# Performance work log

Hardware: AMD Instinct MI355X
Metric: run time of the kernel (lower is better)

The kernel has to match this reference:

```python
import jax, jax.numpy as jnp
import numpy as np

NUM_HEADS = 4
LOCAL_RADIUS = 2


def setup_inputs() -> dict:
    key = jax.random.key(0)
    ks = jax.random.split(key, 7)
    B, C, H, W = 1, 256, 40, 40
    O = 256  # out_channels
    s = 1.0 / np.sqrt(C).astype(np.float32)
    x = jax.random.normal(ks[0], (B, C, H, W), dtype=jnp.float32)
    Wq = jax.random.normal(ks[1], (C, O), dtype=jnp.float32) * s
    Wk = jax.random.normal(ks[2], (C, O), dtype=jnp.float32) * s
    Wv = jax.random.normal(ks[3], (C, O), dtype=jnp.float32) * s
    bq = jnp.zeros((O,), jnp.float32)
    bk = jnp.zeros((O,), jnp.float32)
    bv = jnp.zeros((O,), jnp.float32)
    return {"x": x, "Wq": Wq, "bq": bq, "Wk": Wk, "bk": bk, "Wv": Wv, "bv": bv}


def reference(x, Wq, bq, Wk, bk, Wv, bv):
    B, C, H, W = x.shape
    N = H * W
    O = Wq.shape[1]
    hd = O // NUM_HEADS
    # Faithful to torch: x.view(B, N, -1) is a raw row-major reshape of (B,C,H,W)
    xf = x.reshape(B, N, C)
    # projections -> (B, heads, N, head_dim)
    q = (xf @ Wq + bq).reshape(B, N, NUM_HEADS, hd).transpose(0, 2, 1, 3)
    k = (xf @ Wk + bk).reshape(B, N, NUM_HEADS, hd).transpose(0, 2, 1, 3)
    v = (xf @ Wv + bv).reshape(B, N, NUM_HEADS, hd).transpose(0, 2, 1, 3)
    scale = jnp.asarray(O, jnp.float32) ** 0.5
    acc = jnp.zeros_like(v)
    # 25 shifted full-attention passes; roll is over (heads, points) axes,
    # exactly matching torch key.roll(shifts=(h,w), dims=(-3,-2)).
    for h in range(-LOCAL_RADIUS, LOCAL_RADIUS + 1):
        for w in range(-LOCAL_RADIUS, LOCAL_RADIUS + 1):
            rk = jnp.roll(k, shift=(h, w), axis=(1, 2))
            scores = jnp.einsum('bhnd,bhmd->bhnm', q, rk) / scale  # (B,h,N,N)
            attn = jax.nn.softmax(scores, axis=-1)
            rv = jnp.roll(v, shift=(-h, -w), axis=(1, 2))
            acc = acc + jnp.einsum('bhnm,bhmd->bhnd', attn, rv)
    # (B, heads, N, hd) -> (B, N, O)
    return acc.transpose(0, 2, 1, 3).reshape(B, N, O)
```

## Files before the change

kernel.cpp:

```cpp
#include <hip/hip_runtime.h>
#include <hip/hip_bf16.h>
#include <stdint.h>

typedef __attribute__((ext_vector_type(8))) __bf16 bf16x8;
typedef __attribute__((ext_vector_type(4))) float f32x4;

#define N_PTS 1600
#define HD    64

#define OFF_WT   0u
#define OFF_BIAS 393216u
#define OFF_VHT  394752u
#define OFF_QH   1213952u
#define OFF_KH   2033152u
#define OFF_KF   2852352u
#define OFF_VF   3671552u

__device__ __forceinline__ float bf2f(ushort h) {
  union { uint32_t u; float f; } v; v.u = ((uint32_t)h) << 16; return v.f;
}
__device__ __forceinline__ ushort f2bf(float f) {
  union { float f; uint32_t u; } v; v.f = f;
  uint32_t u = v.u;
  return (ushort)((u + 0x7FFFu + ((u >> 16) & 1u)) >> 16);
}
__device__ __forceinline__ uint32_t pk2(float a, float b) {
  union { __hip_bfloat162 h; uint32_t u; } cv;
  cv.h = __float22bfloat162_rn(make_float2(a, b));
  return cv.u;
}

__device__ __forceinline__ int detect_f32(const ushort* xu, int* shflag) {
  int t = threadIdx.x & 255;
  if (t == 0) *shflag = 0;
  __syncthreads();
  int local = 0;
#pragma unroll
  for (int i = 0; i < 4; ++i) {
    float v = bf2f(xu[(t * 4 + i) * 2]);
    if (!(fabsf(v) < 1e4f)) local = 1;
  }
  if (local) atomicOr(shflag, 1);
  __syncthreads();
  return *shflag;
}

__global__ void k_prep(const void* __restrict__ x, const void* __restrict__ Wq,
                       const void* __restrict__ bq, const void* __restrict__ Wk,
                       const void* __restrict__ bk, const void* __restrict__ Wv,
                       const void* __restrict__ bv, char* __restrict__ ws) {
  __shared__ int shflag;
  __shared__ ushort tileb[32][33];
  int isf32 = detect_f32((const ushort*)x, &shflag);
  int b = blockIdx.x, t = threadIdx.x;

  if (b < 192) {
    int z = b >> 6, tile = b & 63;
    const void* W = (z == 0) ? Wq : ((z == 1) ? Wk : Wv);
    int o0 = (tile & 7) * 32, k0 = (tile >> 3) * 32;
    int tx = t & 31, ty = t >> 5;
#pragma unroll
    for (int i = 0; i < 32; i += 8) {
      int kk = (k0 + ty + i) * 256 + o0 + tx;
      tileb[ty + i][tx] = isf32 ? f2bf(((const float*)W)[kk]) : ((const ushort*)W)[kk];
    }
    __syncthreads();
    ushort* WT = (ushort*)(ws + OFF_WT) + z * 65536;
#pragma unroll
    for (int i = 0; i < 32; i += 8)
      WT[(o0 + ty + i) * 256 + k0 + tx] = tileb[tx][ty + i];
  } else {
    ushort* bb = (ushort*)(ws + OFF_BIAS);
#pragma unroll
    for (int z = 0; z < 3; ++z) {
      const void* B = (z == 0) ? bq : ((z == 1) ? bk : bv);
      bb[z * 256 + t] = isf32 ? f2bf(((const float*)B)[t]) : ((const ushort*)B)[t];
    }
  }
}

__launch_bounds__(256)
__global__ void k_proj(const void* __restrict__ x, const ushort* __restrict__ WT,
                       const ushort* __restrict__ bias3,
                       ushort* __restrict__ Qh, ushort* __restrict__ Kh, ushort* __restrict__ VhT) {
  __shared__ int shflag;
  int isf32 = detect_f32((const ushort*)x, &shflag);
  int z = blockIdx.z;
  const ushort* WTz = WT + z * 65536;
  const ushort* bias = bias3 + z * 256;
  int n0 = blockIdx.x * 16;
  int head = threadIdx.x >> 6;
  int lane = threadIdx.x & 63;
  int c = lane & 15, quad = lane >> 4;

  f32x4 acc[4];
#pragma unroll
  for (int i = 0; i < 4; ++i) acc[i] = (f32x4){0.f, 0.f, 0.f, 0.f};

  int ebase = (n0 + c) * 256;
#pragma unroll
  for (int kt = 0; kt < 8; ++kt) {
    bf16x8 a;
    if (isf32) {
      const float4* X4 = (const float4*)x;
      int i4 = (ebase + kt * 32 + quad * 8) >> 2;
      float4 f0 = X4[i4], f1 = X4[i4 + 1];
      union { ushort us[8]; bf16x8 v; } cv;
      cv.us[0] = f2bf(f0.x); cv.us[1] = f2bf(f0.y);
      cv.us[2] = f2bf(f0.z); cv.us[3] = f2bf(f0.w);
      cv.us[4] = f2bf(f1.x); cv.us[5] = f2bf(f1.y);
      cv.us[6] = f2bf(f1.z); cv.us[7] = f2bf(f1.w);
      a = cv.v;
    } else {
      a = *(const bf16x8*)((const ushort*)x + ebase + kt * 32 + quad * 8);
    }
#pragma unroll
    for (int os = 0; os < 4; ++os) {
      bf16x8 bfr = *(const bf16x8*)(WTz + (head * 64 + os * 16 + c) * 256 + kt * 32 + quad * 8);
      acc[os] = __builtin_amdgcn_mfma_f32_16x16x32_bf16(a, bfr, acc[os], 0, 0, 0);
    }
  }
  if (z == 2) {
#pragma unroll
    for (int os = 0; os < 4; ++os) {
      float bval = bf2f(bias[head * 64 + os * 16 + c]);
      ushort4 v;
      v.x = f2bf(acc[os][0] + bval); v.y = f2bf(acc[os][1] + bval);
      v.z = f2bf(acc[os][2] + bval); v.w = f2bf(acc[os][3] + bval);
      *(ushort4*)(VhT + (head * 64 + os * 16 + c) * N_PTS + n0 + quad * 4) = v;
    }
  } else {
    float scale = (z == 0) ? 0.0625f * 1.44269504088896f : 1.0f;
    ushort* out = (z == 0) ? Qh : Kh;
#pragma unroll
    for (int os = 0; os < 4; ++os) {
      float bval = bf2f(bias[head * 64 + os * 16 + c]);
#pragma unroll
      for (int r = 0; r < 4; ++r)
        out[head * (N_PTS * HD) + (n0 + quad * 4 + r) * HD + os * 16 + c] =
            f2bf((acc[os][r] + bval) * scale);
    }
  }
}

__global__ void k_frag(const ushort* __restrict__ Kh, const ushort* __restrict__ VhT,
                       ushort* __restrict__ Kf, ushort* __restrict__ Vf) {
  int q = blockIdx.x * 256 + threadIdx.x;
  int isV = q >= 51200;
  int idx = isV ? q - 51200 : q;
  int lane = idx & 63, ch = (idx >> 6) & 3;
  int rest = idx >> 8;
  int t = rest % 50, g = rest / 50;
  int c = lane & 15, quad = lane >> 4;
  if (!isV) {
    int perm = ((c >> 2) << 3) + (c & 3);
    int key = t * 32 + perm + ((ch >> 1) << 2);
    int d0 = (ch & 1) * 32 + quad * 8;
    bf16x8 v = *(const bf16x8*)(Kh + (size_t)(g * N_PTS + key) * HD + d0);
    *(bf16x8*)(Kf + (size_t)idx * 8) = v;
  } else {
    int d = ch * 16 + c;
    int m0 = t * 32 + quad * 8;
    const ushort* row = VhT + (size_t)(g * HD + d) * N_PTS;
    int mp = (m0 == 0) ? 1592 : m0 - 8;
    int mn = (m0 == 1592) ? 0 : m0 + 8;
    union { bf16x8 v[3]; ushort us[24]; } w;
    w.v[0] = *(const bf16x8*)(row + mp);
    w.v[1] = *(const bf16x8*)(row + m0);
    w.v[2] = *(const bf16x8*)(row + mn);
    union { ushort us[8]; bf16x8 v; } o;
#pragma unroll
    for (int j = 0; j < 8; ++j) {
      float s = bf2f(w.us[4 + j]) + bf2f(w.us[6 + j]) + bf2f(w.us[8 + j]) +
                bf2f(w.us[10 + j]) + bf2f(w.us[12 + j]);
      o.us[j] = f2bf(s);
    }
    *(bf16x8*)(Vf + (size_t)idx * 8) = o.v;
  }
}

__device__ __forceinline__ bf16x8 pack_p8(const f32x4& s0, const f32x4& s1, float& lp) {
  float e0 = exp2f(s0[0]), e1 = exp2f(s0[1]), e2 = exp2f(s0[2]), e3 = exp2f(s0[3]);
  float e4 = exp2f(s1[0]), e5 = exp2f(s1[1]), e6 = exp2f(s1[2]), e7 = exp2f(s1[3]);
  lp += ((e0 + e1) + (e2 + e3)) + ((e4 + e5) + (e6 + e7));
  union { uint32_t u[4]; bf16x8 v; } r;
  r.u[0] = pk2(e0, e1); r.u[1] = pk2(e2, e3);
  r.u[2] = pk2(e4, e5); r.u[3] = pk2(e6, e7);
  return r.v;
}

#define MFMA16(a, b, cc) __builtin_amdgcn_mfma_f32_16x16x32_bf16(a, b, cc, 0, 0, 0)

#define LOADT(sfx, t) do {                                            \
    const char* kt_ = kfp + (size_t)(t) * 4096;                       \
    const char* vt_ = vfp + (size_t)(t) * 4096;                       \
    ka0##sfx = *(const bf16x8*)(kt_);                                 \
    ka1##sfx = *(const bf16x8*)(kt_ + 1024);                          \
    kb0##sfx = *(const bf16x8*)(kt_ + 2048);                          \
    kb1##sfx = *(const bf16x8*)(kt_ + 3072);                          \
    vb0##sfx = *(const bf16x8*)(vt_);                                 \
    vb1##sfx = *(const bf16x8*)(vt_ + 1024);                          \
    vb2##sfx = *(const bf16x8*)(vt_ + 2048);                          \
    vb3##sfx = *(const bf16x8*)(vt_ + 3072);                          \
  } while (0)

#define COMPUTE(sfx) do {                                             \
    __builtin_amdgcn_s_setprio(1);                                    \
    f32x4 s0 = MFMA16(ka0##sfx, qa00, z4);                            \
    s0 = MFMA16(ka1##sfx, qa01, s0);                                  \
    f32x4 s1 = MFMA16(kb0##sfx, qa00, z4);                            \
    s1 = MFMA16(kb1##sfx, qa01, s1);                                  \
    bf16x8 pa0 = pack_p8(s0, s1, lp0);                                \
    oacc0[0] = MFMA16(pa0, vb0##sfx, oacc0[0]);                       \
    oacc0[1] = MFMA16(pa0, vb1##sfx, oacc0[1]);                       \
    oacc0[2] = MFMA16(pa0, vb2##sfx, oacc0[2]);                       \
    oacc0[3] = MFMA16(pa0, vb3##sfx, oacc0[3]);                       \
    s0 = MFMA16(ka0##sfx, qa10, z4);                                  \
    s0 = MFMA16(ka1##sfx, qa11, s0);                                  \
    s1 = MFMA16(kb0##sfx, qa10, z4);                                  \
    s1 = MFMA16(kb1##sfx, qa11, s1);                                  \
    bf16x8 pa1 = pack_p8(s0, s1, lp1);                                \
    oacc1[0] = MFMA16(pa1, vb0##sfx, oacc1[0]);                       \
    oacc1[1] = MFMA16(pa1, vb1##sfx, oacc1[1]);                       \
    oacc1[2] = MFMA16(pa1, vb2##sfx, oacc1[2]);                       \
    oacc1[3] = MFMA16(pa1, vb3##sfx, oacc1[3]);                       \
    __builtin_amdgcn_s_setprio(0);                                    \
  } while (0)

__launch_bounds__(512)
__global__ void k_attn(const ushort* __restrict__ Qh, const ushort* __restrict__ Kf,
                       const ushort* __restrict__ Vf, const void* __restrict__ x,
                       void* __restrict__ out) {
  __shared__ int shflag;
  __shared__ float obuf[8][16][68];
  __shared__ float lbuf[8][16];
  int isf32 = detect_f32((const ushort*)x, &shflag);

  int qt = blockIdx.x;
  int hp = blockIdx.y;
  int tid = threadIdx.x, sp = tid >> 6, lane = tid & 63;
  int kg = sp & 3, zh = sp >> 2;
  int vg = (2 * hp - kg + 8) & 3;
  int c = lane & 15, quad = lane >> 4;
  int n0 = qt * 16;

  const ushort* q0row = Qh + ((hp    ) * N_PTS + n0 + c) * HD;
  const ushort* q1row = Qh + ((hp + 2) * N_PTS + n0 + c) * HD;
  bf16x8 qa00 = *(const bf16x8*)(q0row + quad * 8);
  bf16x8 qa01 = *(const bf16x8*)(q0row + 32 + quad * 8);
  bf16x8 qa10 = *(const bf16x8*)(q1row + quad * 8);
  bf16x8 qa11 = *(const bf16x8*)(q1row + 32 + quad * 8);

  f32x4 oacc0[4], oacc1[4];
#pragma unroll
  for (int i = 0; i < 4; ++i) {
    oacc0[i] = (f32x4){0.f, 0.f, 0.f, 0.f};
    oacc1[i] = (f32x4){0.f, 0.f, 0.f, 0.f};
  }
  float lp0 = 0.f, lp1 = 0.f;

  int off = zh * 25;
  const int iters = 25;
  const f32x4 z4 = (f32x4){0.f, 0.f, 0.f, 0.f};

  const char* kfp = (const char*)Kf + (size_t)(kg * 50 + off) * 4096 + lane * 16;
  const char* vfp = (const char*)Vf + (size_t)(vg * 50 + off) * 4096 + lane * 16;

  bf16x8 ka0A, ka1A, kb0A, kb1A, vb0A, vb1A, vb2A, vb3A;
  bf16x8 ka0B, ka1B, kb0B, kb1B, vb0B, vb1B, vb2B, vb3B;

  LOADT(A, 0);
  int it = 0;
  for (; it + 2 <= iters; it += 2) {
    LOADT(B, it + 1);
    COMPUTE(A);
    int tn = (it + 2 < iters) ? (it + 2) : (it + 1);
    LOADT(A, tn);
    COMPUTE(B);
  }
  if (it < iters) COMPUTE(A);

  lp0 += __shfl_xor(lp0, 16, 64); lp0 += __shfl_xor(lp0, 32, 64);
  lp1 += __shfl_xor(lp1, 16, 64); lp1 += __shfl_xor(lp1, 32, 64);

#pragma unroll
  for (int h = 0; h < 2; ++h) {
    __syncthreads();
    const f32x4* oa = h ? oacc1 : oacc0;
#pragma unroll
    for (int ds = 0; ds < 4; ++ds)
#pragma unroll
      for (int r = 0; r < 4; ++r)
        obuf[sp][quad * 4 + r][ds * 16 + c] = oa[ds][r];
    if (quad == 0) lbuf[sp][c] = h ? lp1 : lp0;
    __syncthreads();

    int q = tid >> 5, dp = (tid & 31) * 2;
    int hq = hp + 2 * h;
    float a0 = 0.f, a1 = 0.f;
#pragma unroll
    for (int g = 0; g < 4; ++g) {
      float n0v = obuf[g][q][dp]     + obuf[g + 4][q][dp];
      float n1v = obuf[g][q][dp + 1] + obuf[g + 4][q][dp + 1];
      float l   = lbuf[g][q] + lbuf[g + 4][q];
      float w   = (g == ((hq + 2) & 3)) ? 2.f : 1.f;
      float rl  = w / l;
      a0 += n0v * rl; a1 += n1v * rl;
    }
    size_t oidx = (size_t)(n0 + q) * 256 + hq * 64 + dp;
    if (isf32) {
      ((float2*)out)[oidx >> 1] = make_float2(a0, a1);
    } else {
      ((uint32_t*)out)[oidx >> 1] = pk2(a0, a1);
    }
  }
}

extern "C" void kernel_launch(void* const* d_in, const int* in_sizes, int n_in,
                              void* d_out, int out_size, void* d_ws, size_t ws_size,
                              hipStream_t stream) {
  char* ws = (char*)d_ws;
  ushort* WT    = (ushort*)(ws + OFF_WT);
  ushort* bias3 = (ushort*)(ws + OFF_BIAS);
  ushort* VhT   = (ushort*)(ws + OFF_VHT);
  ushort* Qh    = (ushort*)(ws + OFF_QH);
  ushort* Kh    = (ushort*)(ws + OFF_KH);
  ushort* Kf    = (ushort*)(ws + OFF_KF);
  ushort* Vf    = (ushort*)(ws + OFF_VF);

  k_prep<<<193, 256, 0, stream>>>(d_in[0], d_in[1], d_in[2], d_in[3],
                                  d_in[4], d_in[5], d_in[6], ws);
  k_proj<<<dim3(100, 1, 3), 256, 0, stream>>>(d_in[0], WT, bias3, Qh, Kh, VhT);
  k_frag<<<400, 256, 0, stream>>>(Kh, VhT, Kf, Vf);
  k_attn<<<dim3(100, 2), 512, 0, stream>>>(Qh, Kf, Vf, d_in[0], d_out);
}
```

Baseline: 109.4 us.

## Fuse prep, projection, fragment and attention kernels into one cooperative kernel

Replaces four separate kernel launches with a single cooperative launch of 200 blocks of 512 threads, using grid-wide syncs between the weight transpose, QKV projection, K/V fragment reshuffle and attention phases. Each phase's work is remapped onto the fixed grid: 512-thread blocks split into two 256-thread halves for projection jobs, and each block handles 512 fragment elements. This removes launch overheads and inter-kernel gaps. The cost is grid-barrier latency and a larger shared-memory footprint per block, which applies across every phase.

Measured after the change: 192.9 us. 1.76x slower.

```diff
diff --git a/kernel.cpp b/kernel.cpp
--- a/kernel.cpp
+++ b/kernel.cpp
@@ -1,6 +1,9 @@
 #include <hip/hip_runtime.h>
 #include <hip/hip_bf16.h>
+#include <hip/hip_cooperative_groups.h>
 #include <stdint.h>
+
+namespace cg = cooperative_groups;
 
 typedef __attribute__((ext_vector_type(8))) __bf16 bf16x8;
 typedef __attribute__((ext_vector_type(4))) float f32x4;
@@ -43,140 +46,6 @@
   if (local) atomicOr(shflag, 1);
   __syncthreads();
   return *shflag;
-}
-
-__global__ void k_prep(const void* __restrict__ x, const void* __restrict__ Wq,
-                       const void* __restrict__ bq, const void* __restrict__ Wk,
-                       const void* __restrict__ bk, const void* __restrict__ Wv,
-                       const void* __restrict__ bv, char* __restrict__ ws) {
-  __shared__ int shflag;
-  __shared__ ushort tileb[32][33];
-  int isf32 = detect_f32((const ushort*)x, &shflag);
-  int b = blockIdx.x, t = threadIdx.x;
-
-  if (b < 192) {
-    int z = b >> 6, tile = b & 63;
-    const void* W = (z == 0) ? Wq : ((z == 1) ? Wk : Wv);
-    int o0 = (tile & 7) * 32, k0 = (tile >> 3) * 32;
-    int tx = t & 31, ty = t >> 5;
-#pragma unroll
-    for (int i = 0; i < 32; i += 8) {
-      int kk = (k0 + ty + i) * 256 + o0 + tx;
-      tileb[ty + i][tx] = isf32 ? f2bf(((const float*)W)[kk]) : ((const ushort*)W)[kk];
-    }
-    __syncthreads();
-    ushort* WT = (ushort*)(ws + OFF_WT) + z * 65536;
-#pragma unroll
-    for (int i = 0; i < 32; i += 8)
-      WT[(o0 + ty + i) * 256 + k0 + tx] = tileb[tx][ty + i];
-  } else {
-    ushort* bb = (ushort*)(ws + OFF_BIAS);
-#pragma unroll
-    for (int z = 0; z < 3; ++z) {
-      const void* B = (z == 0) ? bq : ((z == 1) ? bk : bv);
-      bb[z * 256 + t] = isf32 ? f2bf(((const float*)B)[t]) : ((const ushort*)B)[t];
-    }
-  }
-}
-
-__launch_bounds__(256)
-__global__ void k_proj(const void* __restrict__ x, const ushort* __restrict__ WT,
-                       const ushort* __restrict__ bias3,
-                       ushort* __restrict__ Qh, ushort* __restrict__ Kh, ushort* __restrict__ VhT) {
-  __shared__ int shflag;
-  int isf32 = detect_f32((const ushort*)x, &shflag);
-  int z = blockIdx.z;
-  const ushort* WTz = WT + z * 65536;
-  const ushort* bias = bias3 + z * 256;
-  int n0 = blockIdx.x * 16;
-  int head = threadIdx.x >> 6;
-  int lane = threadIdx.x & 63;
-  int c = lane & 15, quad = lane >> 4;
-
-  f32x4 acc[4];
-#pragma unroll
-  for (int i = 0; i < 4; ++i) acc[i] = (f32x4){0.f, 0.f, 0.f, 0.f};
-
-  int ebase = (n0 + c) * 256;
-#pragma unroll
-  for (int kt = 0; kt < 8; ++kt) {
-    bf16x8 a;
-    if (isf32) {
-      const float4* X4 = (const float4*)x;
-      int i4 = (ebase + kt * 32 + quad * 8) >> 2;
-      float4 f0 = X4[i4], f1 = X4[i4 + 1];
-      union { ushort us[8]; bf16x8 v; } cv;
-      cv.us[0] = f2bf(f0.x); cv.us[1] = f2bf(f0.y);
-      cv.us[2] = f2bf(f0.z); cv.us[3] = f2bf(f0.w);
-      cv.us[4] = f2bf(f1.x); cv.us[5] = f2bf(f1.y);
-      cv.us[6] = f2bf(f1.z); cv.us[7] = f2bf(f1.w);
-      a = cv.v;
-    } else {
-      a = *(const bf16x8*)((const ushort*)x + ebase + kt * 32 + quad * 8);
-    }
-#pragma unroll
-    for (int os = 0; os < 4; ++os) {
-      bf16x8 bfr = *(const bf16x8*)(WTz + (head * 64 + os * 16 + c) * 256 + kt * 32 + quad * 8);
-      acc[os] = __builtin_amdgcn_mfma_f32_16x16x32_bf16(a, bfr, acc[os], 0, 0, 0);
-    }
-  }
-  if (z == 2) {
-#pragma unroll
-    for (int os = 0; os < 4; ++os) {
-      float bval = bf2f(bias[head * 64 + os * 16 + c]);
-      ushort4 v;
-      v.x = f2bf(acc[os][0] + bval); v.y = f2bf(acc[os][1] + bval);
-      v.z = f2bf(acc[os][2] + bval); v.w = f2bf(acc[os][3] + bval);
-      *(ushort4*)(VhT + (head * 64 + os * 16 + c) * N_PTS + n0 + quad * 4) = v;
-    }
-  } else {
-    float scale = (z == 0) ? 0.0625f * 1.44269504088896f : 1.0f;
-    ushort* out = (z == 0) ? Qh : Kh;
-#pragma unroll
-    for (int os = 0; os < 4; ++os) {
-      float bval = bf2f(bias[head * 64 + os * 16 + c]);
-#pragma unroll
-      for (int r = 0; r < 4; ++r)
-        out[head * (N_PTS * HD) + (n0 + quad * 4 + r) * HD + os * 16 + c] =
-            f2bf((acc[os][r] + bval) * scale);
-    }
-  }
-}
-
-__global__ void k_frag(const ushort* __restrict__ Kh, const ushort* __restrict__ VhT,
-                       ushort* __restrict__ Kf, ushort* __restrict__ Vf) {
-  int q = blockIdx.x * 256 + threadIdx.x;
-  int isV = q >= 51200;
-  int idx = isV ? q - 51200 : q;
-  int lane = idx & 63, ch = (idx >> 6) & 3;
-  int rest = idx >> 8;
-  int t = rest % 50, g = rest / 50;
-  int c = lane & 15, quad = lane >> 4;
-  if (!isV) {
-    int perm = ((c >> 2) << 3) + (c & 3);
-    int key = t * 32 + perm + ((ch >> 1) << 2);
-    int d0 = (ch & 1) * 32 + quad * 8;
-    bf16x8 v = *(const bf16x8*)(Kh + (size_t)(g * N_PTS + key) * HD + d0);
-    *(bf16x8*)(Kf + (size_t)idx * 8) = v;
-  } else {
-    int d = ch * 16 + c;
-    int m0 = t * 32 + quad * 8;
-    const ushort* row = VhT + (size_t)(g * HD + d) * N_PTS;
-    int mp = (m0 == 0) ? 1592 : m0 - 8;
-    int mn = (m0 == 1592) ? 0 : m0 + 8;
-    union { bf16x8 v[3]; ushort us[24]; } w;
-    w.v[0] = *(const bf16x8*)(row + mp);
-    w.v[1] = *(const bf16x8*)(row + m0);
-    w.v[2] = *(const bf16x8*)(row + mn);
-    union { ushort us[8]; bf16x8 v; } o;
-#pragma unroll
-    for (int j = 0; j < 8; ++j) {
-      float s = bf2f(w.us[4 + j]) + bf2f(w.us[6 + j]) + bf2f(w.us[8 + j]) +
-                bf2f(w.us[10 + j]) + bf2f(w.us[12 + j]);
-      o.us[j] = f2bf(s);
-    }
-    *(bf16x8*)(Vf + (size_t)idx * 8) = o.v;
-  }
 }
 
 __device__ __forceinline__ bf16x8 pack_p8(const f32x4& s0, const f32x4& s1, float& lp) {
@@ -228,90 +97,231 @@
   } while (0)
 
 __launch_bounds__(512)
-__global__ void k_attn(const ushort* __restrict__ Qh, const ushort* __restrict__ Kf,
-                       const ushort* __restrict__ Vf, const void* __restrict__ x,
-                       void* __restrict__ out) {
+__global__ void k_fused(const void* __restrict__ x, const void* __restrict__ Wq,
+                        const void* __restrict__ bq, const void* __restrict__ Wk,
+                        const void* __restrict__ bk, const void* __restrict__ Wv,
+                        const void* __restrict__ bv, char* __restrict__ ws,
+                        void* __restrict__ out) {
+  cg::grid_group grid = cg::this_grid();
   __shared__ int shflag;
+  __shared__ ushort tileb[32][33];
   __shared__ float obuf[8][16][68];
   __shared__ float lbuf[8][16];
+
   int isf32 = detect_f32((const ushort*)x, &shflag);
-
-  int qt = blockIdx.x;
-  int hp = blockIdx.y;
-  int tid = threadIdx.x, sp = tid >> 6, lane = tid & 63;
-  int kg = sp & 3, zh = sp >> 2;
-  int vg = (2 * hp - kg + 8) & 3;
-  int c = lane & 15, quad = lane >> 4;
-  int n0 = qt * 16;
-
-  const ushort* q0row = Qh + ((hp    ) * N_PTS + n0 + c) * HD;
-  const ushort* q1row = Qh + ((hp + 2) * N_PTS + n0 + c) * HD;
-  bf16x8 qa00 = *(const bf16x8*)(q0row + quad * 8);
-  bf16x8 qa01 = *(const bf16x8*)(q0row + 32 + quad * 8);
-  bf16x8 qa10 = *(const bf16x8*)(q1row + quad * 8);
-  bf16x8 qa11 = *(const bf16x8*)(q1row + 32 + quad * 8);
-
-  f32x4 oacc0[4], oacc1[4];
-#pragma unroll
-  for (int i = 0; i < 4; ++i) {
-    oacc0[i] = (f32x4){0.f, 0.f, 0.f, 0.f};
-    oacc1[i] = (f32x4){0.f, 0.f, 0.f, 0.f};
-  }
-  float lp0 = 0.f, lp1 = 0.f;
-
-  int off = zh * 25;
-  const int iters = 25;
-  const f32x4 z4 = (f32x4){0.f, 0.f, 0.f, 0.f};
-
-  const char* kfp = (const char*)Kf + (size_t)(kg * 50 + off) * 4096 + lane * 16;
-  const char* vfp = (const char*)Vf + (size_t)(vg * 50 + off) * 4096 + lane * 16;
-
-  bf16x8 ka0A, ka1A, kb0A, kb1A, vb0A, vb1A, vb2A, vb3A;
-  bf16x8 ka0B, ka1B, kb0B, kb1B, vb0B, vb1B, vb2B, vb3B;
-
-  LOADT(A, 0);
-  int it = 0;
-  for (; it + 2 <= iters; it += 2) {
-    LOADT(B, it + 1);
-    COMPUTE(A);
-    int tn = (it + 2 < iters) ? (it + 2) : (it + 1);
-    LOADT(A, tn);
-    COMPUTE(B);
-  }
-  if (it < iters) COMPUTE(A);
-
-  lp0 += __shfl_xor(lp0, 16, 64); lp0 += __shfl_xor(lp0, 32, 64);
-  lp1 += __shfl_xor(lp1, 16, 64); lp1 += __shfl_xor(lp1, 32, 64);
-
-#pragma unroll
-  for (int h = 0; h < 2; ++h) {
+  int b = blockIdx.x, tid = threadIdx.x;
+
+  if (b < 192) {
+    int z = b >> 6, tile = b & 63;
+    const void* W = (z == 0) ? Wq : ((z == 1) ? Wk : Wv);
+    int o0 = (tile & 7) * 32, k0 = (tile >> 3) * 32;
+    int tx = tid & 31, ty = tid >> 5;
+#pragma unroll
+    for (int i = 0; i < 32; i += 16) {
+      int kk = (k0 + ty + i) * 256 + o0 + tx;
+      tileb[ty + i][tx] = isf32 ? f2bf(((const float*)W)[kk]) : ((const ushort*)W)[kk];
+    }
     __syncthreads();
-    const f32x4* oa = h ? oacc1 : oacc0;
-#pragma unroll
-    for (int ds = 0; ds < 4; ++ds)
-#pragma unroll
-      for (int r = 0; r < 4; ++r)
-        obuf[sp][quad * 4 + r][ds * 16 + c] = oa[ds][r];
-    if (quad == 0) lbuf[sp][c] = h ? lp1 : lp0;
-    __syncthreads();
-
-    int q = tid >> 5, dp = (tid & 31) * 2;
-    int hq = hp + 2 * h;
-    float a0 = 0.f, a1 = 0.f;
-#pragma unroll
-    for (int g = 0; g < 4; ++g) {
-      float n0v = obuf[g][q][dp]     + obuf[g + 4][q][dp];
-      float n1v = obuf[g][q][dp + 1] + obuf[g + 4][q][dp + 1];
-      float l   = lbuf[g][q] + lbuf[g + 4][q];
-      float w   = (g == ((hq + 2) & 3)) ? 2.f : 1.f;
-      float rl  = w / l;
-      a0 += n0v * rl; a1 += n1v * rl;
-    }
-    size_t oidx = (size_t)(n0 + q) * 256 + hq * 64 + dp;
-    if (isf32) {
-      ((float2*)out)[oidx >> 1] = make_float2(a0, a1);
+    ushort* WT = (ushort*)(ws + OFF_WT) + z * 65536;
+#pragma unroll
+    for (int i = 0; i < 32; i += 16)
+      WT[(o0 + ty + i) * 256 + k0 + tx] = tileb[tx][ty + i];
+  } else if (b == 192 && tid < 256) {
+    ushort* bb = (ushort*)(ws + OFF_BIAS);
+#pragma unroll
+    for (int z = 0; z < 3; ++z) {
+      const void* B = (z == 0) ? bq : ((z == 1) ? bk : bv);
+      bb[z * 256 + tid] = isf32 ? f2bf(((const float*)B)[tid]) : ((const ushort*)B)[tid];
+    }
+  }
+  grid.sync();
+
+  {
+    int half = tid >> 8;
+    int job = b + 200 * half;
+    if (job < 300) {
+      int z = job / 100;
+      int n0 = (job % 100) * 16;
+      const ushort* WTz = (const ushort*)(ws + OFF_WT) + z * 65536;
+      const ushort* bias = (const ushort*)(ws + OFF_BIAS) + z * 256;
+      int t256 = tid & 255;
+      int head = t256 >> 6, lane = t256 & 63;
+      int c = lane & 15, quad = lane >> 4;
+
+      f32x4 acc[4];
+#pragma unroll
+      for (int i = 0; i < 4; ++i) acc[i] = (f32x4){0.f, 0.f, 0.f, 0.f};
+
+      int ebase = (n0 + c) * 256;
+#pragma unroll
+      for (int kt = 0; kt < 8; ++kt) {
+        bf16x8 a;
+        if (isf32) {
+          const float4* X4 = (const float4*)x;
+          int i4 = (ebase + kt * 32 + quad * 8) >> 2;
+          float4 f0 = X4[i4], f1 = X4[i4 + 1];
+          union { ushort us[8]; bf16x8 v; } cv;
+          cv.us[0] = f2bf(f0.x); cv.us[1] = f2bf(f0.y);
+          cv.us[2] = f2bf(f0.z); cv.us[3] = f2bf(f0.w);
+          cv.us[4] = f2bf(f1.x); cv.us[5] = f2bf(f1.y);
+          cv.us[6] = f2bf(f1.z); cv.us[7] = f2bf(f1.w);
+          a = cv.v;
+        } else {
+          a = *(const bf16x8*)((const ushort*)x + ebase + kt * 32 + quad * 8);
+        }
+#pragma unroll
+        for (int os = 0; os < 4; ++os) {
+          bf16x8 bfr = *(const bf16x8*)(WTz + (head * 64 + os * 16 + c) * 256 + kt * 32 + quad * 8);
+          acc[os] = __builtin_amdgcn_mfma_f32_16x16x32_bf16(a, bfr, acc[os], 0, 0, 0);
+        }
+      }
+      if (z == 2) {
+        ushort* VhT = (ushort*)(ws + OFF_VHT);
+#pragma unroll
+        for (int os = 0; os < 4; ++os) {
+          float bval = bf2f(bias[head * 64 + os * 16 + c]);
+          ushort4 v;
+          v.x = f2bf(acc[os][0] + bval); v.y = f2bf(acc[os][1] + bval);
+          v.z = f2bf(acc[os][2] + bval); v.w = f2bf(acc[os][3] + bval);
+          *(ushort4*)(VhT + (head * 64 + os * 16 + c) * N_PTS + n0 + quad * 4) = v;
+        }
+      } else {
+        float scale = (z == 0) ? 0.0625f * 1.44269504088896f : 1.0f;
+        ushort* o = (ushort*)(ws + ((z == 0) ? OFF_QH : OFF_KH));
+#pragma unroll
+        for (int os = 0; os < 4; ++os) {
+          float bval = bf2f(bias[head * 64 + os * 16 + c]);
+#pragma unroll
+          for (int r = 0; r < 4; ++r)
+            o[head * (N_PTS * HD) + (n0 + quad * 4 + r) * HD + os * 16 + c] =
+                f2bf((acc[os][r] + bval) * scale);
+        }
+      }
+    }
+  }
+  grid.sync();
+
+  {
+    const ushort* Kh = (const ushort*)(ws + OFF_KH);
+    const ushort* VhT = (const ushort*)(ws + OFF_VHT);
+    ushort* Kf = (ushort*)(ws + OFF_KF);
+    ushort* Vf = (ushort*)(ws + OFF_VF);
+    int q = b * 512 + tid;
+    int isV = q >= 51200;
+    int idx = isV ? q - 51200 : q;
+    int lane = idx & 63, ch = (idx >> 6) & 3;
+    int rest = idx >> 8;
+    int t = rest % 50, g = rest / 50;
+    int c = lane & 15, quad = lane >> 4;
+    if (!isV) {
+      int perm = ((c >> 2) << 3) + (c & 3);
+      int key = t * 32 + perm + ((ch >> 1) << 2);
+      int d0 = (ch & 1) * 32 + quad * 8;
+      bf16x8 v = *(const bf16x8*)(Kh + (size_t)(g * N_PTS + key) * HD + d0);
+      *(bf16x8*)(Kf + (size_t)idx * 8) = v;
     } else {
-      ((uint32_t*)out)[oidx >> 1] = pk2(a0, a1);
+      int d = ch * 16 + c;
+      int m0 = t * 32 + quad * 8;
+      const ushort* row = VhT + (size_t)(g * HD + d) * N_PTS;
+      int mp = (m0 == 0) ? 1592 : m0 - 8;
+      int mn = (m0 == 1592) ? 0 : m0 + 8;
+      union { bf16x8 v[3]; ushort us[24]; } w;
+      w.v[0] = *(const bf16x8*)(row + mp);
+      w.v[1] = *(const bf16x8*)(row + m0);
+      w.v[2] = *(const bf16x8*)(row + mn);
+      union { ushort us[8]; bf16x8 v; } o;
+#pragma unroll
+      for (int j = 0; j < 8; ++j) {
+        float s = bf2f(w.us[4 + j]) + bf2f(w.us[6 + j]) + bf2f(w.us[8 + j]) +
+                  bf2f(w.us[10 + j]) + bf2f(w.us[12 + j]);
+        o.us[j] = f2bf(s);
+      }
+      *(bf16x8*)(Vf + (size_t)idx * 8) = o.v;
+    }
+  }
+  grid.sync();
+
+  {
+    const ushort* Qh = (const ushort*)(ws + OFF_QH);
+    const char* Kf = (const char*)(ws + OFF_KF);
+    const char* Vf = (const char*)(ws + OFF_VF);
+    int hp = (b >= 100) ? 1 : 0;
+    int qt = b - hp * 100;
+    int sp = tid >> 6, lane = tid & 63;
+    int kg = sp & 3, zh = sp >> 2;
+    int vg = (2 * hp - kg + 8) & 3;
+    int c = lane & 15, quad = lane >> 4;
+    int n0 = qt * 16;
+
+    const ushort* q0row = Qh + ((hp    ) * N_PTS + n0 + c) * HD;
+    const ushort* q1row = Qh + ((hp + 2) * N_PTS + n0 + c) * HD;
+    bf16x8 qa00 = *(const bf16x8*)(q0row + quad * 8);
+    bf16x8 qa01 = *(const bf16x8*)(q0row + 32 + quad * 8);
+    bf16x8 qa10 = *(const bf16x8*)(q1row + quad * 8);
+    bf16x8 qa11 = *(const bf16x8*)(q1row + 32 + quad * 8);
+
+    f32x4 oacc0[4], oacc1[4];
+#pragma unroll
+    for (int i = 0; i < 4; ++i) {
+      oacc0[i] = (f32x4){0.f, 0.f, 0.f, 0.f};
+      oacc1[i] = (f32x4){0.f, 0.f, 0.f, 0.f};
+    }
+    float lp0 = 0.f, lp1 = 0.f;
+
+    int off = zh * 25;
+    const int iters = 25;
+    const f32x4 z4 = (f32x4){0.f, 0.f, 0.f, 0.f};
+
+    const char* kfp = Kf + (size_t)(kg * 50 + off) * 4096 + lane * 16;
+    const char* vfp = Vf + (size_t)(vg * 50 + off) * 4096 + lane * 16;
+
+    bf16x8 ka0A, ka1A, kb0A, kb1A, vb0A, vb1A, vb2A, vb3A;
+    bf16x8 ka0B, ka1B, kb0B, kb1B, vb0B, vb1B, vb2B, vb3B;
+
+    LOADT(A, 0);
+    int it = 0;
+    for (; it + 2 <= iters; it += 2) {
+      LOADT(B, it + 1);
+      COMPUTE(A);
+      int tn = (it + 2 < iters) ? (it + 2) : (it + 1);
+      LOADT(A, tn);
+      COMPUTE(B);
+    }
+    if (it < iters) COMPUTE(A);
+
+    lp0 += __shfl_xor(lp0, 16, 64); lp0 += __shfl_xor(lp0, 32, 64);
+    lp1 += __shfl_xor(lp1, 16, 64); lp1 += __shfl_xor(lp1, 32, 64);
+
+#pragma unroll
+    for (int h = 0; h < 2; ++h) {
+      __syncthreads();
+      const f32x4* oa = h ? oacc1 : oacc0;
+#pragma unroll
+      for (int ds = 0; ds < 4; ++ds)
+#pragma unroll
+        for (int r = 0; r < 4; ++r)
+          obuf[sp][quad * 4 + r][ds * 16 + c] = oa[ds][r];
+      if (quad == 0) lbuf[sp][c] = h ? lp1 : lp0;
+      __syncthreads();
+
+      int q = tid >> 5, dp = (tid & 31) * 2;
+      int hq = hp + 2 * h;
+      float a0 = 0.f, a1 = 0.f;
+#pragma unroll
+      for (int g = 0; g < 4; ++g) {
+        float n0v = obuf[g][q][dp]     + obuf[g + 4][q][dp];
+        float n1v = obuf[g][q][dp + 1] + obuf[g + 4][q][dp + 1];
+        float l   = lbuf[g][q] + lbuf[g + 4][q];
+        float w   = (g == ((hq + 2) & 3)) ? 2.f : 1.f;
+        float rl  = w / l;
+        a0 += n0v * rl; a1 += n1v * rl;
+      }
+      size_t oidx = (size_t)(n0 + q) * 256 + hq * 64 + dp;
+      if (isf32) {
+        ((float2*)out)[oidx >> 1] = make_float2(a0, a1);
+      } else {
+        ((uint32_t*)out)[oidx >> 1] = pk2(a0, a1);
+      }
     }
   }
 }
@@ -319,18 +329,16 @@
 extern "C" void kernel_launch(void* const* d_in, const int* in_sizes, int n_in,
                               void* d_out, int out_size, void* d_ws, size_t ws_size,
                               hipStream_t stream) {
+  const void* x  = d_in[0];
+  const void* Wq = d_in[1];
+  const void* bq = d_in[2];
+  const void* Wk = d_in[3];
+  const void* bk = d_in[4];
+  const void* Wv = d_in[5];
+  const void* bv = d_in[6];
   char* ws = (char*)d_ws;
-  ushort* WT    = (ushort*)(ws + OFF_WT);
-  ushort* bias3 = (ushort*)(ws + OFF_BIAS);
-  ushort* VhT   = (ushort*)(ws + OFF_VHT);
-  ushort* Qh    = (ushort*)(ws + OFF_QH);
-  ushort* Kh    = (ushort*)(ws + OFF_KH);
-  ushort* Kf    = (ushort*)(ws + OFF_KF);
-  ushort* Vf    = (ushort*)(ws + OFF_VF);
-
-  k_prep<<<193, 256, 0, stream>>>(d_in[0], d_in[1], d_in[2], d_in[3],
-                                  d_in[4], d_in[5], d_in[6], ws);
-  k_proj<<<dim3(100, 1, 3), 256, 0, stream>>>(d_in[0], WT, bias3, Qh, Kh, VhT);
-  k_frag<<<400, 256, 0, stream>>>(Kh, VhT, Kf, Vf);
-  k_attn<<<dim3(100, 2), 512, 0, stream>>>(Qh, Kf, Vf, d_in[0], d_out);
-}
+  void* outp = d_out;
+  void* args[] = {(void*)&x, (void*)&Wq, (void*)&bq, (void*)&Wk, (void*)&bk,
+                  (void*)&Wv, (void*)&bv, (void*)&ws, (void*)&outp};
+  hipLaunchCooperativeKernel((void*)k_fused, dim3(200), dim3(512), args, 0, stream);
+}
```

## Fuse weight prep and K fragment layout into projection kernel

Applied to the files above, without the earlier changes.

Removes the separate weight-transpose/bias prep kernel by reading the weights directly (with on-the-fly bf16 conversion) inside the projection kernel. The K fragment permutation is now done through shared memory in the projection epilogue, and only the V fragment kernel remains. This cuts two launches and the intermediate Kh/WT buffers, at the cost of strided, uncoalesced weight loads per MFMA fragment in the projection.

Result: slower. 161.4 us (+47.6%).

```diff
diff --git a/kernel.cpp b/kernel.cpp
--- a/kernel.cpp
+++ b/kernel.cpp
@@ -8,13 +8,10 @@
 #define N_PTS 1600
 #define HD    64
 
-#define OFF_WT   0u
-#define OFF_BIAS 393216u
-#define OFF_VHT  394752u
-#define OFF_QH   1213952u
-#define OFF_KH   2033152u
-#define OFF_KF   2852352u
-#define OFF_VF   3671552u
+#define OFF_VHT  0u
+#define OFF_QH   819200u
+#define OFF_KF   1638400u
+#define OFF_VF   2457600u
 
 __device__ __forceinline__ float bf2f(ushort h) {
   union { uint32_t u; float f; } v; v.u = ((uint32_t)h) << 16; return v.f;
@@ -45,52 +42,23 @@
   return *shflag;
 }
 
-__global__ void k_prep(const void* __restrict__ x, const void* __restrict__ Wq,
+__launch_bounds__(512)
+__global__ void k_proj(const void* __restrict__ x, const void* __restrict__ Wq,
                        const void* __restrict__ bq, const void* __restrict__ Wk,
                        const void* __restrict__ bk, const void* __restrict__ Wv,
                        const void* __restrict__ bv, char* __restrict__ ws) {
   __shared__ int shflag;
-  __shared__ ushort tileb[32][33];
+  __shared__ ushort ktile[2][4][16][72];
   int isf32 = detect_f32((const ushort*)x, &shflag);
-  int b = blockIdx.x, t = threadIdx.x;
-
-  if (b < 192) {
-    int z = b >> 6, tile = b & 63;
-    const void* W = (z == 0) ? Wq : ((z == 1) ? Wk : Wv);
-    int o0 = (tile & 7) * 32, k0 = (tile >> 3) * 32;
-    int tx = t & 31, ty = t >> 5;
-#pragma unroll
-    for (int i = 0; i < 32; i += 8) {
-      int kk = (k0 + ty + i) * 256 + o0 + tx;
-      tileb[ty + i][tx] = isf32 ? f2bf(((const float*)W)[kk]) : ((const ushort*)W)[kk];
-    }
-    __syncthreads();
-    ushort* WT = (ushort*)(ws + OFF_WT) + z * 65536;
-#pragma unroll
-    for (int i = 0; i < 32; i += 8)
-      WT[(o0 + ty + i) * 256 + k0 + tx] = tileb[tx][ty + i];
-  } else {
-    ushort* bb = (ushort*)(ws + OFF_BIAS);
-#pragma unroll
-    for (int z = 0; z < 3; ++z) {
-      const void* B = (z == 0) ? bq : ((z == 1) ? bk : bv);
-      bb[z * 256 + t] = isf32 ? f2bf(((const float*)B)[t]) : ((const ushort*)B)[t];
-    }
-  }
-}
-
-__launch_bounds__(256)
-__global__ void k_proj(const void* __restrict__ x, const ushort* __restrict__ WT,
-                       const ushort* __restrict__ bias3,
-                       ushort* __restrict__ Qh, ushort* __restrict__ Kh, ushort* __restrict__ VhT) {
-  __shared__ int shflag;
-  int isf32 = detect_f32((const ushort*)x, &shflag);
-  int z = blockIdx.z;
-  const ushort* WTz = WT + z * 65536;
-  const ushort* bias = bias3 + z * 256;
-  int n0 = blockIdx.x * 16;
-  int head = threadIdx.x >> 6;
-  int lane = threadIdx.x & 63;
+  int tid = threadIdx.x;
+  int half = tid >> 8;
+  int job = blockIdx.x + 150 * half;
+  int z = job / 100, nb = job % 100;
+  int n0 = nb * 16;
+  const void* W = (z == 0) ? Wq : ((z == 1) ? Wk : Wv);
+  const void* B = (z == 0) ? bq : ((z == 1) ? bk : bv);
+  int t256 = tid & 255;
+  int head = t256 >> 6, lane = t256 & 63;
   int c = lane & 15, quad = lane >> 4;
 
   f32x4 acc[4];
@@ -116,67 +84,89 @@
     }
 #pragma unroll
     for (int os = 0; os < 4; ++os) {
-      bf16x8 bfr = *(const bf16x8*)(WTz + (head * 64 + os * 16 + c) * 256 + kt * 32 + quad * 8);
-      acc[os] = __builtin_amdgcn_mfma_f32_16x16x32_bf16(a, bfr, acc[os], 0, 0, 0);
-    }
-  }
-  if (z == 2) {
+      int row = head * 64 + os * 16 + c;
+      union { ushort us[8]; bf16x8 v; } bfr;
+#pragma unroll
+      for (int j = 0; j < 8; ++j) {
+        int kk = (kt * 32 + quad * 8 + j) * 256 + row;
+        bfr.us[j] = isf32 ? f2bf(((const float*)W)[kk]) : ((const ushort*)W)[kk];
+      }
+      acc[os] = __builtin_amdgcn_mfma_f32_16x16x32_bf16(a, bfr.v, acc[os], 0, 0, 0);
+    }
+  }
+
+  float scale = (z == 0) ? 0.0625f * 1.44269504088896f : 1.0f;
+  if (z != 2) {
 #pragma unroll
     for (int os = 0; os < 4; ++os) {
-      float bval = bf2f(bias[head * 64 + os * 16 + c]);
+      int row = head * 64 + os * 16 + c;
+      ushort bu = isf32 ? f2bf(((const float*)B)[row]) : ((const ushort*)B)[row];
+      float bval = bf2f(bu);
+#pragma unroll
+      for (int r = 0; r < 4; ++r)
+        ktile[half][head][quad * 4 + r][os * 16 + c] = f2bf((acc[os][r] + bval) * scale);
+    }
+  } else {
+    ushort* VhT = (ushort*)(ws + OFF_VHT);
+#pragma unroll
+    for (int os = 0; os < 4; ++os) {
+      int row = head * 64 + os * 16 + c;
+      ushort bu = isf32 ? f2bf(((const float*)B)[row]) : ((const ushort*)B)[row];
+      float bval = bf2f(bu);
       ushort4 v;
       v.x = f2bf(acc[os][0] + bval); v.y = f2bf(acc[os][1] + bval);
       v.z = f2bf(acc[os][2] + bval); v.w = f2bf(acc[os][3] + bval);
-      *(ushort4*)(VhT + (head * 64 + os * 16 + c) * N_PTS + n0 + quad * 4) = v;
-    }
-  } else {
-    float scale = (z == 0) ? 0.0625f * 1.44269504088896f : 1.0f;
-    ushort* out = (z == 0) ? Qh : Kh;
-#pragma unroll
-    for (int os = 0; os < 4; ++os) {
-      float bval = bf2f(bias[head * 64 + os * 16 + c]);
-#pragma unroll
-      for (int r = 0; r < 4; ++r)
-        out[head * (N_PTS * HD) + (n0 + quad * 4 + r) * HD + os * 16 + c] =
-            f2bf((acc[os][r] + bval) * scale);
-    }
-  }
-}
-
-__global__ void k_frag(const ushort* __restrict__ Kh, const ushort* __restrict__ VhT,
-                       ushort* __restrict__ Kf, ushort* __restrict__ Vf) {
-  int q = blockIdx.x * 256 + threadIdx.x;
-  int isV = q >= 51200;
-  int idx = isV ? q - 51200 : q;
+      *(ushort4*)(VhT + (size_t)row * N_PTS + n0 + quad * 4) = v;
+    }
+  }
+  __syncthreads();
+
+  if (z == 0) {
+    ushort* Qh = (ushort*)(ws + OFF_QH);
+    int kl = lane >> 2, d0 = (lane & 3) * 16;
+    bf16x8 v0 = *(const bf16x8*)&ktile[half][head][kl][d0];
+    bf16x8 v1 = *(const bf16x8*)&ktile[half][head][kl][d0 + 8];
+    ushort* qrow = Qh + (size_t)head * (N_PTS * HD) + (size_t)(n0 + kl) * HD + d0;
+    *(bf16x8*)qrow = v0;
+    *(bf16x8*)(qrow + 8) = v1;
+  } else if (z == 1) {
+    ushort* Kf = (ushort*)(ws + OFF_KF);
+    int hf = nb & 1, t = nb >> 1;
+    int quad_o = lane >> 4, chp = (lane >> 3) & 1, cc = (lane & 7) + hf * 8;
+#pragma unroll
+    for (int e = 0; e < 2; ++e) {
+      int ch = chp + 2 * e;
+      int kl = ((cc >> 2) << 3) + (cc & 3) + ((ch >> 1) << 2) - hf * 16;
+      int d0 = (ch & 1) * 32 + quad_o * 8;
+      bf16x8 v = *(const bf16x8*)&ktile[half][head][kl][d0];
+      *(bf16x8*)(Kf + ((((size_t)head * 50 + t) * 4 + ch) * 64 + quad_o * 16 + cc) * 8) = v;
+    }
+  }
+}
+
+__global__ void k_fragV(const ushort* __restrict__ VhT, ushort* __restrict__ Vf) {
+  int idx = blockIdx.x * 512 + threadIdx.x;
   int lane = idx & 63, ch = (idx >> 6) & 3;
   int rest = idx >> 8;
   int t = rest % 50, g = rest / 50;
   int c = lane & 15, quad = lane >> 4;
-  if (!isV) {
-    int perm = ((c >> 2) << 3) + (c & 3);
-    int key = t * 32 + perm + ((ch >> 1) << 2);
-    int d0 = (ch & 1) * 32 + quad * 8;
-    bf16x8 v = *(const bf16x8*)(Kh + (size_t)(g * N_PTS + key) * HD + d0);
-    *(bf16x8*)(Kf + (size_t)idx * 8) = v;
-  } else {
-    int d = ch * 16 + c;
-    int m0 = t * 32 + quad * 8;
-    const ushort* row = VhT + (size_t)(g * HD + d) * N_PTS;
-    int mp = (m0 == 0) ? 1592 : m0 - 8;
-    int mn = (m0 == 1592) ? 0 : m0 + 8;
-    union { bf16x8 v[3]; ushort us[24]; } w;
-    w.v[0] = *(const bf16x8*)(row + mp);
-    w.v[1] = *(const bf16x8*)(row + m0);
-    w.v[2] = *(const bf16x8*)(row + mn);
-    union { ushort us[8]; bf16x8 v; } o;
-#pragma unroll
-    for (int j = 0; j < 8; ++j) {
-      float s = bf2f(w.us[4 + j]) + bf2f(w.us[6 + j]) + bf2f(w.us[8 + j]) +
-                bf2f(w.us[10 + j]) + bf2f(w.us[12 + j]);
-      o.us[j] = f2bf(s);
-    }
-    *(bf16x8*)(Vf + (size_t)idx * 8) = o.v;
-  }
+  int d = ch * 16 + c;
+  int m0 = t * 32 + quad * 8;
+  const ushort* row = VhT + (size_t)(g * HD + d) * N_PTS;
+  int mp = (m0 == 0) ? 1592 : m0 - 8;
+  int mn = (m0 == 1592) ? 0 : m0 + 8;
+  union { bf16x8 v[3]; ushort us[24]; } w;
+  w.v[0] = *(const bf16x8*)(row + mp);
+  w.v[1] = *(const bf16x8*)(row + m0);
+  w.v[2] = *(const bf16x8*)(row + mn);
+  union { ushort us[8]; bf16x8 v; } o;
+#pragma unroll
+  for (int j = 0; j < 8; ++j) {
+    float s = bf2f(w.us[4 + j]) + bf2f(w.us[6 + j]) + bf2f(w.us[8 + j]) +
+              bf2f(w.us[10 + j]) + bf2f(w.us[12 + j]);
+    o.us[j] = f2bf(s);
+  }
+  *(bf16x8*)(Vf + (size_t)idx * 8) = o.v;
 }
 
 __device__ __forceinline__ bf16x8 pack_p8(const f32x4& s0, const f32x4& s1, float& lp) {
@@ -320,17 +310,13 @@
                               void* d_out, int out_size, void* d_ws, size_t ws_size,
                               hipStream_t stream) {
   char* ws = (char*)d_ws;
-  ushort* WT    = (ushort*)(ws + OFF_WT);
-  ushort* bias3 = (ushort*)(ws + OFF_BIAS);
-  ushort* VhT   = (ushort*)(ws + OFF_VHT);
-  ushort* Qh    = (ushort*)(ws + OFF_QH);
-  ushort* Kh    = (ushort*)(ws + OFF_KH);
-  ushort* Kf    = (ushort*)(ws + OFF_KF);
-  ushort* Vf    = (ushort*)(ws + OFF_VF);
-
-  k_prep<<<193, 256, 0, stream>>>(d_in[0], d_in[1], d_in[2], d_in[3],
+  ushort* VhT = (ushort*)(ws + OFF_VHT);
+  ushort* Qh  = (ushort*)(ws + OFF_QH);
+  ushort* Kf  = (ushort*)(ws + OFF_KF);
+  ushort* Vf  = (ushort*)(ws + OFF_VF);
+
+  k_proj<<<150, 512, 0, stream>>>(d_in[0], d_in[1], d_in[2], d_in[3],
                                   d_in[4], d_in[5], d_in[6], ws);
-  k_proj<<<dim3(100, 1, 3), 256, 0, stream>>>(d_in[0], WT, bias3, Qh, Kh, VhT);
-  k_frag<<<400, 256, 0, stream>>>(Kh, VhT, Kf, Vf);
+  k_fragV<<<100, 512, 0, stream>>>(VhT, Vf);
   k_attn<<<dim3(100, 2), 512, 0, stream>>>(Qh, Kf, Vf, d_in[0], d_out);
 }
```
